# Kernel optimization log

Measured on AMD Instinct MI355X. Metric: run time of the kernel, lower is better.

Reference implementation:

```python
import jax, jax.numpy as jnp
import numpy as np

B, T, IN, OUT = 32, 2048, 1024, 256
DT = 1.0
TAU_MIN, TAU_MAX = 15.0, 25.0


def setup_inputs() -> dict:
    key = jax.random.key(0)
    k1, k2, k3 = jax.random.split(key, 3)
    inputs = jax.random.normal(k1, (B, T, IN), dtype=jnp.float32)
    bound = float(np.sqrt(1.0 / IN))
    weight = jax.random.uniform(k2, (OUT, IN), minval=-bound, maxval=bound, dtype=jnp.float32)
    bias = jnp.zeros((OUT,), dtype=jnp.float32)
    tau = jax.random.uniform(k3, (OUT,), minval=TAU_MIN, maxval=TAU_MAX, dtype=jnp.float32)
    decay = jnp.exp(-DT / tau)  # per-channel leak alpha in (0,1)
    return {"inputs": inputs, "weight": weight, "bias": bias, "decay": decay}


def reference(inputs, weight, bias, decay):
    # Dense projection: [B,T,IN] @ [IN,OUT] -> [B,T,OUT]
    current = jnp.einsum("bti,oi->bto", inputs, weight) + bias
    # Leaky integrator: u_t = alpha * u_{t-1} + (1-alpha) * x_t, u_0 = 0
    one_minus = 1.0 - decay

    def step(u, x):  # u,x: [B,OUT]
        u = decay * u + one_minus * x
        return u, u

    u0 = jnp.zeros((inputs.shape[0], weight.shape[0]), dtype=current.dtype)
    _, us = jax.lax.scan(step, u0, jnp.swapaxes(current, 0, 1))  # [T,B,OUT]
    return jnp.swapaxes(us, 0, 1)  # [B,T,OUT]
```

## Files before the change

### kernel.cpp

```cpp
#include <hip/hip_runtime.h>

#define B_   32
#define T_   2048
#define IN_  1024
#define OUT_ 256
#define M_   (B_ * T_)

#define BM 128
#define BN 256
#define BK 32
#define NSTEPS (IN_ / BK)
#define THREADS 512

#define LC 32
#define NC (T_ / LC)
#define XPAD 264

#define SMEM_BYTES (BM * XPAD * 2)
#define ABUF_OFF(c) ((c) * (BM * BK * 2))
#define BBUF_OFF(c) (2 * (BM * BK * 2) + (c) * (BN * BK * 2))

typedef __attribute__((ext_vector_type(4))) float f32x4;
typedef __attribute__((ext_vector_type(8))) __bf16 bf16x8;

__device__ __forceinline__ unsigned int f2bf_pk(float a, float b) {
    unsigned int ua = __float_as_uint(a);
    unsigned int ub = __float_as_uint(b);
    ua = (ua + 0x7fffu + ((ua >> 16) & 1u)) >> 16;
    ub = (ub + 0x7fffu + ((ub >> 16) & 1u)) >> 16;
    return ua | (ub << 16);
}
__device__ __forceinline__ unsigned short f2bf1(float a) {
    unsigned int ua = __float_as_uint(a);
    return (unsigned short)((ua + 0x7fffu + ((ua >> 16) & 1u)) >> 16);
}
__device__ __forceinline__ float bf2f(unsigned short s) {
    return __uint_as_float((unsigned int)s << 16);
}

__device__ __forceinline__ void gload_lds16(const void* g, void* l) {
    __builtin_amdgcn_global_load_lds(
        (const __attribute__((address_space(1))) void*)g,
        (__attribute__((address_space(3))) void*)l, 16, 0, 0);
}

__global__ __launch_bounds__(256) void convert_w(const float* __restrict__ W,
                                                 unsigned short* __restrict__ Wb) {
    const int i = blockIdx.x * 256 + threadIdx.x;
    const float4 v = ((const float4*)W)[i];
    uint2 o;
    o.x = f2bf_pk(v.x, v.y);
    o.y = f2bf_pk(v.z, v.w);
    ((uint2*)Wb)[i] = o;
}

__global__ __launch_bounds__(THREADS, 4) void gemm_fused(
    const float* __restrict__ A, const unsigned short* __restrict__ Wb,
    const float* __restrict__ bias, const float* __restrict__ decay,
    unsigned short* __restrict__ Xb, float* __restrict__ chunkend) {
    __shared__ __align__(16) char smem[SMEM_BYTES];

    const int tid  = threadIdx.x;
    const int lane = tid & 63;
    const int wid  = tid >> 6;
    const int wm   = wid >> 2;
    const int wn   = wid & 3;
    const int l15  = lane & 15;
    const int l4   = lane >> 4;
    const int bm0  = blockIdx.x * BM;

    const int rowA = tid >> 2;
    const int gA   = tid & 3;
    const float* gsrcA = A + (size_t)(bm0 + rowA) * IN_ + gA * 8;
    const int ldsA = rowA * BK + ((gA ^ (rowA & 3)) << 3);

    const unsigned short* gsrcB[2];
    int ldsBbase[2];
#pragma unroll
    for (int i = 0; i < 2; ++i) {
        const int q = (wid + i * 8) * 64 + lane;
        const int r = q >> 2;
        const int g = (q & 3) ^ (r & 3);
        gsrcB[i] = Wb + (size_t)r * IN_ + g * 8;
        ldsBbase[i] = (wid + i * 8) * 1024;
    }

    f32x4 acc[4][4] = {};
    float4 a0, a1;

#pragma unroll
    for (int i = 0; i < 2; ++i)
        gload_lds16(gsrcB[i], smem + BBUF_OFF(0) + ldsBbase[i]);
    a0 = *(const float4*)(gsrcA);
    a1 = *(const float4*)(gsrcA + 4);
    {
        int4 w;
        w.x = f2bf_pk(a0.x, a0.y); w.y = f2bf_pk(a0.z, a0.w);
        w.z = f2bf_pk(a1.x, a1.y); w.w = f2bf_pk(a1.z, a1.w);
        *(int4*)(smem + ABUF_OFF(0) + ldsA * 2) = w;
    }
    __syncthreads();

    int cur = 0;
    for (int step = 0; step < NSTEPS; ++step) {
        const int nxt = step + 1;
        if (nxt < NSTEPS) {
            const int k0 = nxt * BK;
#pragma unroll
            for (int i = 0; i < 2; ++i)
                gload_lds16(gsrcB[i] + k0, smem + BBUF_OFF(cur ^ 1) + ldsBbase[i]);
            a0 = *(const float4*)(gsrcA + k0);
            a1 = *(const float4*)(gsrcA + k0 + 4);
        }
        {
            const unsigned short* Ab = (const unsigned short*)(smem + ABUF_OFF(cur));
            const unsigned short* Bb = (const unsigned short*)(smem + BBUF_OFF(cur));
            bf16x8 af[4], bfv[4];
#pragma unroll
            for (int mi = 0; mi < 4; ++mi) {
                const int row = wm * 64 + mi * 16 + l15;
                af[mi] = *(const bf16x8*)&Ab[row * BK + ((l4 ^ (row & 3)) << 3)];
            }
#pragma unroll
            for (int ni = 0; ni < 4; ++ni) {
                const int col = wn * 64 + ni * 16 + l15;
                bfv[ni] = *(const bf16x8*)&Bb[col * BK + ((l4 ^ (col & 3)) << 3)];
            }
#pragma unroll
            for (int mi = 0; mi < 4; ++mi)
#pragma unroll
                for (int ni = 0; ni < 4; ++ni)
                    acc[mi][ni] = __builtin_amdgcn_mfma_f32_16x16x32_bf16(
                        af[mi], bfv[ni], acc[mi][ni], 0, 0, 0);
        }
        if (nxt < NSTEPS) {
            int4 w;
            w.x = f2bf_pk(a0.x, a0.y); w.y = f2bf_pk(a0.z, a0.w);
            w.z = f2bf_pk(a1.x, a1.y); w.w = f2bf_pk(a1.z, a1.w);
            *(int4*)(smem + ABUF_OFF(cur ^ 1) + ldsA * 2) = w;
        }
        __syncthreads();
        cur ^= 1;
    }

    unsigned short* xt = (unsigned short*)smem;
#pragma unroll
    for (int ni = 0; ni < 4; ++ni) {
        const int col = wn * 64 + ni * 16 + l15;
        const float bv = bias[col];
#pragma unroll
        for (int mi = 0; mi < 4; ++mi) {
            const int r0 = wm * 64 + mi * 16 + (l4 << 2);
#pragma unroll
            for (int r = 0; r < 4; ++r)
                xt[(r0 + r) * XPAD + col] = f2bf1(acc[mi][ni][r] + bv);
        }
    }
    __syncthreads();

    const int b  = bm0 >> 11;
    const int c0 = (bm0 >> 5) & 63;

    {
        const int cr = tid >> 5;
        const int cg = (tid & 31) << 3;
#pragma unroll
        for (int it = 0; it < 8; ++it) {
            const int row = it * 16 + cr;
            bf16x8 v = *(const bf16x8*)&xt[row * XPAD + cg];
            *(bf16x8*)&Xb[(size_t)(bm0 + row) * OUT_ + cg] = v;
        }
    }

    for (int task = tid; task < 4 * OUT_; task += THREADS) {
        const int cl  = task >> 8;
        const int col = task & 255;
        const float alpha = decay[col];
        const float om = 1.0f - alpha;
        float u = 0.0f;
        const unsigned short* p = &xt[(cl * LC) * XPAD + col];
#pragma unroll
        for (int t = 0; t < LC; ++t)
            u = fmaf(alpha, u, om * bf2f(p[t * XPAD]));
        chunkend[(size_t)(b * NC + c0 + cl) * OUT_ + col] = u;
    }
}

__global__ __launch_bounds__(OUT_) void carry_pass(const float* __restrict__ chunkend,
                                                   const float* __restrict__ decay,
                                                   float* __restrict__ carryin) {
    const int b = blockIdx.x;
    const int o = threadIdx.x;
    const float alpha = decay[o];
    float aL = alpha;
#pragma unroll
    for (int i = 1; i < LC; ++i) aL *= alpha;

    float ce[NC];
#pragma unroll
    for (int c = 0; c < NC; ++c)
        ce[c] = chunkend[(size_t)(b * NC + c) * OUT_ + o];

    float carry = 0.0f;
#pragma unroll
    for (int c = 0; c < NC; ++c) {
        carryin[(size_t)(b * NC + c) * OUT_ + o] = carry;
        carry = fmaf(aL, carry, ce[c]);
    }
}

__global__ __launch_bounds__(256) void scan_final(const unsigned short* __restrict__ Xb,
                                                  const float* __restrict__ decay,
                                                  const float* __restrict__ carryin,
                                                  float* __restrict__ out) {
    const int unit = blockIdx.x * 4 + (threadIdx.x >> 6);
    const int l    = threadIdx.x & 63;
    const int col  = l << 2;
    const int b    = unit >> 6;
    const int c    = unit & 63;

    const float4 al = *(const float4*)&decay[col];
    const float4 om = {1.0f - al.x, 1.0f - al.y, 1.0f - al.z, 1.0f - al.w};
    float4 u = *(const float4*)&carryin[(size_t)unit * OUT_ + col];

    const size_t base = (size_t)(b * T_ + c * LC) * OUT_ + col;
#pragma unroll 8
    for (int t = 0; t < LC; ++t) {
        const ushort4 xv = *(const ushort4*)&Xb[base + (size_t)t * OUT_];
        u.x = fmaf(al.x, u.x, om.x * bf2f(xv.x));
        u.y = fmaf(al.y, u.y, om.y * bf2f(xv.y));
        u.z = fmaf(al.z, u.z, om.z * bf2f(xv.z));
        u.w = fmaf(al.w, u.w, om.w * bf2f(xv.w));
        *(float4*)&out[base + (size_t)t * OUT_] = u;
    }
}

__global__ __launch_bounds__(256) void gemm_bias(const float* __restrict__ A,
                                                 const float* __restrict__ W,
                                                 const float* __restrict__ bias,
                                                 float* __restrict__ C) {
    __shared__ float As[16][64 + 4];
    __shared__ float Ws[16][64 + 4];
    const int bm = blockIdx.y * 64;
    const int bn = blockIdx.x * 64;
    const int tid = threadIdx.x;
    const int tx = tid & 15, ty = tid >> 4;
    const int lr = tid >> 2, lc = (tid & 3) << 2;
    float acc[4][4] = {};
    const float* Ap = A + (size_t)(bm + lr) * IN_ + lc;
    const float* Wp = W + (size_t)(bn + lr) * IN_ + lc;
    for (int k0 = 0; k0 < IN_; k0 += 16) {
        const float4 a = *(const float4*)(Ap + k0);
        const float4 w = *(const float4*)(Wp + k0);
        __syncthreads();
        As[lc + 0][lr] = a.x; As[lc + 1][lr] = a.y; As[lc + 2][lr] = a.z; As[lc + 3][lr] = a.w;
        Ws[lc + 0][lr] = w.x; Ws[lc + 1][lr] = w.y; Ws[lc + 2][lr] = w.z; Ws[lc + 3][lr] = w.w;
        __syncthreads();
#pragma unroll
        for (int kk = 0; kk < 16; ++kk) {
            const float4 av = *(const float4*)&As[kk][ty << 2];
            const float4 wv = *(const float4*)&Ws[kk][tx << 2];
            const float a0[4] = {av.x, av.y, av.z, av.w};
            const float w0[4] = {wv.x, wv.y, wv.z, wv.w};
#pragma unroll
            for (int i = 0; i < 4; ++i)
#pragma unroll
                for (int j = 0; j < 4; ++j) acc[i][j] = fmaf(a0[i], w0[j], acc[i][j]);
        }
    }
#pragma unroll
    for (int i = 0; i < 4; ++i) {
        const size_t row = (size_t)(bm + (ty << 2) + i);
#pragma unroll
        for (int j = 0; j < 4; ++j)
            C[row * OUT_ + bn + (tx << 2) + j] = acc[i][j] + bias[bn + (tx << 2) + j];
    }
}

__global__ __launch_bounds__(OUT_) void scan_simple(float* __restrict__ C,
                                                    const float* __restrict__ decay) {
    const int b = blockIdx.x;
    const int o = threadIdx.x;
    const float alpha = decay[o];
    const float om = 1.0f - alpha;
    float u = 0.0f;
    float* p = C + (size_t)b * T_ * OUT_ + o;
    for (int t = 0; t < T_; ++t) {
        const float x = p[(size_t)t * OUT_];
        u = fmaf(alpha, u, om * x);
        p[(size_t)t * OUT_] = u;
    }
}

extern "C" void kernel_launch(void* const* d_in, const int* in_sizes, int n_in,
                              void* d_out, int out_size, void* d_ws, size_t ws_size,
                              hipStream_t stream) {
    const float* inputs = (const float*)d_in[0];
    const float* weight = (const float*)d_in[1];
    const float* bias   = (const float*)d_in[2];
    const float* decay  = (const float*)d_in[3];
    float* out = (float*)d_out;

    const size_t wb_bytes = (size_t)OUT_ * IN_ * 2;
    const size_t ce_bytes = (size_t)B_ * NC * OUT_ * 4;
    const size_t ci_bytes = ce_bytes;
    const size_t x_bytes  = (size_t)M_ * OUT_ * 2;
    const size_t need = wb_bytes + ce_bytes + ci_bytes + x_bytes;

    if (ws_size >= need) {
        char* w = (char*)d_ws;
        unsigned short* Wb = (unsigned short*)w;
        float* chunkend    = (float*)(w + wb_bytes);
        float* carryin     = (float*)(w + wb_bytes + ce_bytes);
        unsigned short* Xb = (unsigned short*)(w + wb_bytes + ce_bytes + ci_bytes);

        convert_w<<<(OUT_ * IN_ / 4) / 256, 256, 0, stream>>>(weight, Wb);
        gemm_fused<<<M_ / BM, THREADS, 0, stream>>>(inputs, Wb, bias, decay, Xb, chunkend);
        carry_pass<<<B_, OUT_, 0, stream>>>(chunkend, decay, carryin);
        scan_final<<<(B_ * NC) / 4, 256, 0, stream>>>(Xb, decay, carryin, out);
    } else {
        dim3 g(OUT_ / 64, M_ / 64);
        gemm_bias<<<g, 256, 0, stream>>>(inputs, weight, bias, out);
        scan_simple<<<B_, OUT_, 0, stream>>>(out, decay);
    }
}
```

Before: 114.1 us.

## Triple-buffer GEMM main loop with depth-two prefetch and explicit waitcnts

Moves the projection GEMM's K loop from double buffering to a three-stage LDS ring. B tiles for step i+2 are issued as direct-to-LDS loads while step i computes, and A fp32 loads run two steps ahead. The loop uses explicit vmcnt/lgkmcnt waits and a raw s_barrier instead of __syncthreads, so memory latency has more time to hide. In exchange LDS use grows slightly, and correctness now depends on the hand-tuned wait counts.

```diff
diff --git a/kernel.cpp b/kernel.cpp
--- a/kernel.cpp
+++ b/kernel.cpp
@@ -16,9 +16,9 @@
 #define NC (T_ / LC)
 #define XPAD 264
 
-#define SMEM_BYTES (BM * XPAD * 2)
 #define ABUF_OFF(c) ((c) * (BM * BK * 2))
-#define BBUF_OFF(c) (2 * (BM * BK * 2) + (c) * (BN * BK * 2))
+#define BBUF_OFF(c) (3 * (BM * BK * 2) + (c) * (BN * BK * 2))
+#define SMEM_BYTES (3 * (BM * BK * 2) + 3 * (BN * BK * 2))
 
 typedef __attribute__((ext_vector_type(4))) float f32x4;
 typedef __attribute__((ext_vector_type(8))) __bf16 bf16x8;
@@ -88,9 +88,8 @@
     f32x4 acc[4][4] = {};
     float4 a0, a1;
 
-#pragma unroll
-    for (int i = 0; i < 2; ++i)
-        gload_lds16(gsrcB[i], smem + BBUF_OFF(0) + ldsBbase[i]);
+    gload_lds16(gsrcB[0], smem + BBUF_OFF(0) + ldsBbase[0]);
+    gload_lds16(gsrcB[1], smem + BBUF_OFF(0) + ldsBbase[1]);
     a0 = *(const float4*)(gsrcA);
     a1 = *(const float4*)(gsrcA + 4);
     {
@@ -99,22 +98,43 @@
         w.z = f2bf_pk(a1.x, a1.y); w.w = f2bf_pk(a1.z, a1.w);
         *(int4*)(smem + ABUF_OFF(0) + ldsA * 2) = w;
     }
-    __syncthreads();
-
-    int cur = 0;
-    for (int step = 0; step < NSTEPS; ++step) {
-        const int nxt = step + 1;
-        if (nxt < NSTEPS) {
-            const int k0 = nxt * BK;
-#pragma unroll
-            for (int i = 0; i < 2; ++i)
-                gload_lds16(gsrcB[i] + k0, smem + BBUF_OFF(cur ^ 1) + ldsBbase[i]);
+    a0 = *(const float4*)(gsrcA + BK);
+    a1 = *(const float4*)(gsrcA + BK + 4);
+    asm volatile("s_waitcnt lgkmcnt(0)" ::: "memory");
+    __builtin_amdgcn_s_barrier();
+    __builtin_amdgcn_sched_barrier(0);
+    gload_lds16(gsrcB[0] + BK, smem + BBUF_OFF(1) + ldsBbase[0]);
+    gload_lds16(gsrcB[1] + BK, smem + BBUF_OFF(1) + ldsBbase[1]);
+
+    for (int i = 0; i < NSTEPS; ++i) {
+        if (i + 1 < NSTEPS) {
+            asm volatile("s_waitcnt vmcnt(2)" ::: "memory");
+        } else {
+            asm volatile("s_waitcnt vmcnt(0)" ::: "memory");
+        }
+        __builtin_amdgcn_sched_barrier(0);
+        if (i + 1 < NSTEPS) {
+            int4 w;
+            w.x = f2bf_pk(a0.x, a0.y); w.y = f2bf_pk(a0.z, a0.w);
+            w.z = f2bf_pk(a1.x, a1.y); w.w = f2bf_pk(a1.z, a1.w);
+            *(int4*)(smem + ABUF_OFF((i + 1) % 3) + ldsA * 2) = w;
+        }
+        if (i + 2 < NSTEPS) {
+            const int k0 = (i + 2) * BK;
             a0 = *(const float4*)(gsrcA + k0);
             a1 = *(const float4*)(gsrcA + k0 + 4);
         }
+        asm volatile("s_waitcnt lgkmcnt(0)" ::: "memory");
+        __builtin_amdgcn_s_barrier();
+        __builtin_amdgcn_sched_barrier(0);
+        if (i + 2 < NSTEPS) {
+            const int k0 = (i + 2) * BK;
+            gload_lds16(gsrcB[0] + k0, smem + BBUF_OFF((i + 2) % 3) + ldsBbase[0]);
+            gload_lds16(gsrcB[1] + k0, smem + BBUF_OFF((i + 2) % 3) + ldsBbase[1]);
+        }
         {
-            const unsigned short* Ab = (const unsigned short*)(smem + ABUF_OFF(cur));
-            const unsigned short* Bb = (const unsigned short*)(smem + BBUF_OFF(cur));
+            const unsigned short* Ab = (const unsigned short*)(smem + ABUF_OFF(i % 3));
+            const unsigned short* Bb = (const unsigned short*)(smem + BBUF_OFF(i % 3));
             bf16x8 af[4], bfv[4];
 #pragma unroll
             for (int mi = 0; mi < 4; ++mi) {
@@ -133,15 +153,8 @@
                     acc[mi][ni] = __builtin_amdgcn_mfma_f32_16x16x32_bf16(
                         af[mi], bfv[ni], acc[mi][ni], 0, 0, 0);
         }
-        if (nxt < NSTEPS) {
-            int4 w;
-            w.x = f2bf_pk(a0.x, a0.y); w.y = f2bf_pk(a0.z, a0.w);
-            w.z = f2bf_pk(a1.x, a1.y); w.w = f2bf_pk(a1.z, a1.w);
-            *(int4*)(smem + ABUF_OFF(cur ^ 1) + ldsA * 2) = w;
-        }
-        __syncthreads();
-        cur ^= 1;
-    }
+    }
+    __syncthreads();
 
     unsigned short* xt = (unsigned short*)smem;
 #pragma unroll
```

After: 114.9 us. About the same (+0.7%).
